# Performance work log

Measured on AMD Instinct MI355X. Metric: run time of the kernel, lower is better.

Reference implementation:

```python
import jax, jax.numpy as jnp
import numpy as np

RADIUS = 0.25
N_SAMPLE = 4096
N_NEIGHBOR = 32
OFF = 512   # voxel-coordinate offset so hashed coords are non-negative
M = 1024    # per-axis range of the voxel hash


def _bin_map():
    # 3^3 = 27 neighbor voxel offsets in {-1,0,1}^3 (Point2Voxel.extract_bin for D=3)
    g = np.stack(np.meshgrid(*([[-1, 0, 1]] * 3), indexing='ij'), -1).reshape(-1, 3)
    return jnp.asarray(g, dtype=jnp.int32)


def _hash(k):
    # k: [..., 3] int32 voxel coords -> unique int32 key (fits: 1024^3 < 2^31)
    return ((k[..., 0] + OFF) * M + (k[..., 1] + OFF)) * M + (k[..., 2] + OFF)


def setup_inputs() -> dict:
    key = jax.random.key(0)
    k1, k2 = jax.random.split(key)
    pos = jax.random.normal(k1, (8, 100000, 3), jnp.float32)
    feat = jax.random.normal(k2, (8, 100000, 64), jnp.float32)
    return {"pos": pos, "feat": feat}


def _graph_one(pos_b, rk):
    """Voxel-hash based neighbor sampling for one point cloud [N,3]."""
    N = pos_b.shape[0]
    vox = jnp.floor(pos_b / RADIUS).astype(jnp.int32)          # [N,3] voxel keys
    hkeys = _hash(vox)                                          # [N]
    order = jnp.argsort(hkeys)                                  # sort points by voxel (hash table)
    skeys = hkeys[order]
    kc, kn = jax.random.split(rk)
    centers = jax.random.randint(kc, (N_SAMPLE,), 0, N)         # sampled center point ids
    nk = _hash(vox[centers][:, None, :] + _bin_map()[None])     # [S,27] neighbor voxel keys
    lo = jnp.searchsorted(skeys, nk, side='left')               # bucket start  [S,27]
    hi = jnp.searchsorted(skeys, nk, side='right')              # bucket end    [S,27]
    counts = hi - lo                                            # bucket sizes
    cum = jnp.cumsum(counts, axis=1)                            # [S,27]
    total = cum[:, -1]                                          # candidates per center (>=1)
    # sample N_NEIGHBOR candidate slots uniformly over all neighbor-voxel points
    r = jax.random.randint(kn, (N_SAMPLE, N_NEIGHBOR), 0, 1 << 30) % total[:, None]
    slot = (r[:, :, None] >= cum[:, None, :]).sum(-1)           # which of the 27 voxels
    cum_ex = jnp.concatenate([jnp.zeros_like(cum[:, :1]), cum[:, :-1]], axis=1)
    prev = jnp.take_along_axis(cum_ex, slot, axis=1)
    start = jnp.take_along_axis(lo, slot, axis=1)
    src = order[start + (r - prev)]                             # [S,K] source point ids
    return centers, src


def reference(pos, feat):
    B, N, D = pos.shape
    C = feat.shape[-1]
    rks = jax.random.split(jax.random.key(42), B)
    centers, src = jax.vmap(_graph_one)(pos, rks)               # [B,S], [B,S,K]
    bidx = jnp.arange(B)[:, None]
    center_flag = jnp.zeros((B, N), pos.dtype).at[bidx, centers].set(1.0)
    src_flag = jnp.zeros((B, N), pos.dtype).at[bidx, src.reshape(B, -1)].set(1.0)
    b3 = jnp.arange(B)[:, None, None]
    pos_src = pos[b3, src]                                      # [B,S,K,3] gather
    pos_ctr = pos[bidx, centers]                                # [B,S,3]
    rel = pos_src - pos_ctr[:, :, None, :]                      # edge geometry
    f_src = feat[b3, src]                                       # [B,S,K,C] gather
    out = jnp.concatenate([rel, f_src], axis=-1)                # [B,S,K,3+C]
    return out, src, centers, center_flag, src_flag
```

## Files before the change

### kernel.cpp

```cpp
#include <hip/hip_runtime.h>
#include <stdint.h>

#define NB 8
#define NPTS 100000
#define NS 4096
#define NN 32
#define NCH 64
#define TLG 17
#define TSLOTS (1 << TLG)
#define TMASK (TSLOTS - 1)

#define OUT_MAIN 0ull
#define OUT_SRC  70254592ull
#define OUT_CTR  71303168ull
#define OUT_CF   71335936ull
#define OUT_SF   72135936ull

__host__ __device__ static inline uint32_t rotl32(uint32_t v, int d) {
    return (v << d) | (v >> (32 - d));
}

__host__ __device__ static inline void tf2x32(uint32_t k0, uint32_t k1,
                                              uint32_t x0, uint32_t x1,
                                              uint32_t& o0, uint32_t& o1) {
    uint32_t ks2 = k0 ^ k1 ^ 0x1BD11BDAu;
    x0 += k0; x1 += k1;
    x0 += x1; x1 = rotl32(x1, 13); x1 ^= x0;
    x0 += x1; x1 = rotl32(x1, 15); x1 ^= x0;
    x0 += x1; x1 = rotl32(x1, 26); x1 ^= x0;
    x0 += x1; x1 = rotl32(x1, 6);  x1 ^= x0;
    x0 += k1; x1 += ks2 + 1u;
    x0 += x1; x1 = rotl32(x1, 17); x1 ^= x0;
    x0 += x1; x1 = rotl32(x1, 29); x1 ^= x0;
    x0 += x1; x1 = rotl32(x1, 16); x1 ^= x0;
    x0 += x1; x1 = rotl32(x1, 24); x1 ^= x0;
    x0 += ks2; x1 += k0 + 2u;
    x0 += x1; x1 = rotl32(x1, 13); x1 ^= x0;
    x0 += x1; x1 = rotl32(x1, 15); x1 ^= x0;
    x0 += x1; x1 = rotl32(x1, 26); x1 ^= x0;
    x0 += x1; x1 = rotl32(x1, 6);  x1 ^= x0;
    x0 += k0; x1 += k1 + 3u;
    x0 += x1; x1 = rotl32(x1, 17); x1 ^= x0;
    x0 += x1; x1 = rotl32(x1, 29); x1 ^= x0;
    x0 += x1; x1 = rotl32(x1, 16); x1 ^= x0;
    x0 += x1; x1 = rotl32(x1, 24); x1 ^= x0;
    x0 += k1; x1 += ks2 + 4u;
    x0 += x1; x1 = rotl32(x1, 13); x1 ^= x0;
    x0 += x1; x1 = rotl32(x1, 15); x1 ^= x0;
    x0 += x1; x1 = rotl32(x1, 26); x1 ^= x0;
    x0 += x1; x1 = rotl32(x1, 6);  x1 ^= x0;
    x0 += ks2; x1 += k0 + 5u;
    o0 = x0; o1 = x1;
}

struct RngKeys {
    uint32_t c0[NB], c1[NB];
    uint32_t n0[NB], n1[NB];
};

__device__ static inline uint32_t pbits32(uint32_t k0, uint32_t k1, uint32_t u) {
    uint32_t o0, o1;
    tf2x32(k0, k1, 0u, u, o0, o1);
    return o0 ^ o1;
}

__device__ static inline int voxhash(const float* __restrict__ p) {
    int vx = (int)floorf(p[0] * 4.0f);
    int vy = (int)floorf(p[1] * 4.0f);
    int vz = (int)floorf(p[2] * 4.0f);
    return ((vx + 512) << 20) | ((vy + 512) << 10) | (vz + 512);
}

__device__ static inline int hslot(int hk) {
    return (int)(((uint32_t)hk * 2654435761u) >> (32 - TLG)) & TMASK;
}

__global__ void k_zero(int* __restrict__ tab_key, int* __restrict__ tab_cnt,
                       int* __restrict__ bctr, float4* __restrict__ flags4) {
    int t = blockIdx.x * blockDim.x + threadIdx.x;
    tab_key[t] = -1;
    tab_cnt[t] = 0;
    if (t < (2 * NB * NPTS) / 4) flags4[t] = make_float4(0.f, 0.f, 0.f, 0.f);
    if (t < NB) bctr[t] = 0;
}

__global__ void k_insert(const float* __restrict__ pos,
                         int* __restrict__ tab_key, int* __restrict__ tab_cnt,
                         int* __restrict__ slotOf) {
    int t = blockIdx.x * blockDim.x + threadIdx.x;
    int b = t / NPTS;
    int hk = voxhash(pos + (size_t)t * 3);
    int base = b << TLG;
    int slot = hslot(hk);
    while (true) {
        int prev = atomicCAS(&tab_key[base + slot], -1, hk);
        if (prev == -1 || prev == hk) break;
        slot = (slot + 1) & TMASK;
    }
    slotOf[t] = slot;
    atomicAdd(&tab_cnt[base + slot], 1);
}

__global__ void k_starts(int* __restrict__ tab_cnt, int* __restrict__ tab_start,
                         int* __restrict__ bctr) {
    __shared__ int sdata[256];
    __shared__ int sbase;
    int t = blockIdx.x * blockDim.x + threadIdx.x;
    int tid = threadIdx.x;
    int b = t >> TLG;
    int c = tab_cnt[t];
    sdata[tid] = c;
    __syncthreads();
    for (int off = 1; off < 256; off <<= 1) {
        int x = (tid >= off) ? sdata[tid - off] : 0;
        __syncthreads();
        sdata[tid] += x;
        __syncthreads();
    }
    if (tid == 255) sbase = atomicAdd(&bctr[b], sdata[255]);
    __syncthreads();
    if (c > 0) {
        tab_start[t] = sbase + sdata[tid] - c;
        tab_cnt[t] = 0;
    }
}

__global__ void k_scatter(const int* __restrict__ slotOf, int* __restrict__ tab_cnt,
                          const int* __restrict__ tab_start, int* __restrict__ listA) {
    int t = blockIdx.x * blockDim.x + threadIdx.x;
    int b = t / NPTS, i = t - b * NPTS;
    int slot = (b << TLG) + slotOf[t];
    int a = atomicAdd(&tab_cnt[slot], 1);
    listA[(size_t)b * NPTS + tab_start[slot] + a] = i;
}

__global__ void k_rank(const int* __restrict__ slotOf,
                       const int* __restrict__ tab_cnt, const int* __restrict__ tab_start,
                       const int* __restrict__ listA, int* __restrict__ listB) {
    int t = blockIdx.x * blockDim.x + threadIdx.x;
    int b = t / NPTS, i = t - b * NPTS;
    int slot = (b << TLG) + slotOf[t];
    int s0 = tab_start[slot];
    int c = tab_cnt[slot];
    const int* L = listA + (size_t)b * NPTS + s0;
    int rank = 0;
    for (int k = 0; k < c; k++) rank += (L[k] < i) ? 1 : 0;
    listB[(size_t)b * NPTS + s0 + rank] = i;
}

__global__ void k_binsel(RngKeys keys, const float* __restrict__ pos,
                         const int* __restrict__ tab_key, const int* __restrict__ tab_cnt,
                         const int* __restrict__ tab_start,
                         int* __restrict__ centers_ws,
                         int* __restrict__ lo_ws, int* __restrict__ cnt_ws,
                         float* __restrict__ out_ctr, float* __restrict__ out_cf) {
    int t = blockIdx.x * blockDim.x + threadIdx.x;
    int bin = t % 27;
    int bs = t / 27;
    int b = bs >> 12, s = bs & (NS - 1);
    uint32_t lower = pbits32(keys.c0[b], keys.c1[b], (uint32_t)s);
    int c = (int)(lower % 100000u);
    const float* p = pos + ((size_t)b * NPTS + c) * 3;
    int hk = voxhash(p) + ((bin / 9) - 1) * (1 << 20)
                        + (((bin / 3) % 3) - 1) * (1 << 10)
                        + ((bin % 3) - 1);
    int base = b << TLG;
    int slot = hslot(hk);
    int lo = 0, cnt = 0;
    while (true) {
        int k = tab_key[base + slot];
        if (k == hk) { lo = tab_start[base + slot]; cnt = tab_cnt[base + slot]; break; }
        if (k == -1) break;
        slot = (slot + 1) & TMASK;
    }
    lo_ws[t] = lo;
    cnt_ws[t] = cnt;
    if (bin == 13) {
        centers_ws[bs] = c;
        out_ctr[bs] = (float)c;
        out_cf[(size_t)b * NPTS + c] = 1.0f;
    }
}

__global__ void k_cumsel(RngKeys keys, const int* __restrict__ listB,
                         const int* __restrict__ lo_ws, const int* __restrict__ cnt_ws,
                         int* __restrict__ src_ws,
                         float* __restrict__ out_src, float* __restrict__ out_sf) {
    __shared__ int scnt[216];
    __shared__ int slo[216];
    int tid = threadIdx.x;
    int base216 = blockIdx.x * 216;
    if (tid < 216) {
        scnt[tid] = cnt_ws[base216 + tid];
        slo[tid]  = lo_ws[base216 + tid];
    }
    __syncthreads();
    if (tid < 8) {
        int* a = scnt + tid * 27;
        int acc = 0;
        for (int i = 0; i < 27; i++) { acc += a[i]; a[i] = acc; }
    }
    __syncthreads();
    int g = tid >> 5, n = tid & 31;
    int bs = blockIdx.x * 8 + g;
    int b = bs >> 12, s = bs & (NS - 1);
    uint32_t lower = pbits32(keys.n0[b], keys.n1[b], (uint32_t)(s * NN + n));
    const int* cum = scnt + g * 27;
    int total = cum[26];
    int r = (int)(lower & 0x3FFFFFFFu) % total;
    int slot = 0, prev = 0;
    #pragma unroll
    for (int i = 0; i < 27; i++) {
        int ci = cum[i];
        if (r >= ci) { slot = i + 1; prev = ci; }
    }
    int pos_in = slo[g * 27 + slot] + (r - prev);
    int src = listB[(size_t)b * NPTS + pos_in];
    int oi = bs * NN + n;
    src_ws[oi] = src;
    out_src[oi] = (float)src;
    out_sf[(size_t)b * NPTS + src] = 1.0f;
}

__global__ void k_gather(const float* __restrict__ pos, const float* __restrict__ feat,
                         const int* __restrict__ centers_ws, const int* __restrict__ src_ws,
                         float* __restrict__ out) {
    __shared__ float sbuf[16 * 67];
    int t = threadIdx.x;
    int g = t >> 4, q = t & 15;
    long long row0 = (long long)blockIdx.x * 16;
    long long row = row0 + g;
    int b = (int)(row >> 17);
    int u = (int)(row & (NS * NN - 1));
    int s = u >> 5;
    int src = src_ws[row];
    const float4 fv = *(const float4*)(feat + ((size_t)b * NPTS + src) * NCH + 4 * q);
    float* sb = sbuf + g * 67;
    sb[3 + 4 * q + 0] = fv.x;
    sb[3 + 4 * q + 1] = fv.y;
    sb[3 + 4 * q + 2] = fv.z;
    sb[3 + 4 * q + 3] = fv.w;
    if (q < 3) {
        int ctr = centers_ws[b * NS + s];
        sb[q] = pos[((size_t)b * NPTS + src) * 3 + q]
              - pos[((size_t)b * NPTS + ctr) * 3 + q];
    }
    __syncthreads();
    float4* ob = (float4*)(out + (size_t)row0 * 67);
    const float4* sv = (const float4*)sbuf;
    ob[t] = sv[t];
    if (t < 12) ob[256 + t] = sv[256 + t];
}

extern "C" void kernel_launch(void* const* d_in, const int* in_sizes, int n_in,
                              void* d_out, int out_size, void* d_ws, size_t ws_size,
                              hipStream_t stream) {
    (void)in_sizes; (void)n_in; (void)out_size; (void)ws_size;
    const float* pos = (const float*)d_in[0];
    const float* feat = (const float*)d_in[1];
    float* out = (float*)d_out;

    RngKeys keys;
    for (int b = 0; b < NB; b++) {
        uint32_t rk0, rk1, kc0, kc1, kn0, kn1;
        tf2x32(0u, 42u, 0u, (uint32_t)b, rk0, rk1);
        tf2x32(rk0, rk1, 0u, 0u, kc0, kc1);
        tf2x32(rk0, rk1, 0u, 1u, kn0, kn1);
        tf2x32(kc0, kc1, 0u, 1u, keys.c0[b], keys.c1[b]);
        tf2x32(kn0, kn1, 0u, 1u, keys.n0[b], keys.n1[b]);
    }

    int* tab_key    = (int*)d_ws;
    int* tab_cnt    = tab_key + (size_t)NB * TSLOTS;
    int* tab_start  = tab_cnt + (size_t)NB * TSLOTS;
    int* bctr       = tab_start + (size_t)NB * TSLOTS;
    int* slotOf     = bctr + NB;
    int* listA      = slotOf + (size_t)NB * NPTS;
    int* listB      = listA + (size_t)NB * NPTS;
    int* lo_ws      = listB + (size_t)NB * NPTS;
    int* cnt_ws     = lo_ws + (size_t)NB * NS * 27;
    int* centers_ws = cnt_ws + (size_t)NB * NS * 27;
    int* src_ws     = centers_ws + (size_t)NB * NS;

    k_zero   <<<(NB * TSLOTS) / 256, 256, 0, stream>>>(tab_key, tab_cnt, bctr,
                                                       (float4*)(out + OUT_CF));
    k_insert <<<(NB * NPTS) / 256, 256, 0, stream>>>(pos, tab_key, tab_cnt, slotOf);
    k_starts <<<(NB * TSLOTS) / 256, 256, 0, stream>>>(tab_cnt, tab_start, bctr);
    k_scatter<<<(NB * NPTS) / 256, 256, 0, stream>>>(slotOf, tab_cnt, tab_start, listA);
    k_rank   <<<(NB * NPTS) / 256, 256, 0, stream>>>(slotOf, tab_cnt, tab_start,
                                                     listA, listB);
    k_binsel <<<(NB * NS * 27) / 256, 256, 0, stream>>>(keys, pos, tab_key, tab_cnt,
                                                        tab_start, centers_ws,
                                                        lo_ws, cnt_ws,
                                                        out + OUT_CTR, out + OUT_CF);
    k_cumsel <<<(NB * NS) / 8, 256, 0, stream>>>(keys, listB, lo_ws, cnt_ws,
                                                 src_ws, out + OUT_SRC, out + OUT_SF);
    k_gather <<<(NB * NS * NN) / 16, 256, 0, stream>>>(pos, feat, centers_ws, src_ws, out);
}
```

Baseline: 417.0 us.

## Fuse bin lookup into neighbor selection and widen gather with nontemporal stores

The hash-bin lookup kernel and the cumulative-selection kernel are merged into one kernel. Each 32-lane group now probes the 27 neighbor voxels itself, keeps the counts and starts in shared memory, and takes the prefix inline, so the lo/cnt workspace round trip and one launch go away. The gather kernel now handles 32 rows per 512-thread block and writes its output with nontemporal stores, aiming to reduce cache pollution from the large streaming write. In exchange, each thread in the fused kernel recomputes the running sum over 27 entries.

```diff
diff --git a/kernel.cpp b/kernel.cpp
--- a/kernel.cpp
+++ b/kernel.cpp
@@ -15,6 +15,8 @@
 #define OUT_CTR  71303168ull
 #define OUT_CF   71335936ull
 #define OUT_SF   72135936ull
+
+typedef float f32x4 __attribute__((ext_vector_type(4)));
 
 __host__ __device__ static inline uint32_t rotl32(uint32_t v, int d) {
     return (v << d) | (v >> (32 - d));
@@ -148,73 +150,56 @@
     listB[(size_t)b * NPTS + s0 + rank] = i;
 }
 
-__global__ void k_binsel(RngKeys keys, const float* __restrict__ pos,
-                         const int* __restrict__ tab_key, const int* __restrict__ tab_cnt,
-                         const int* __restrict__ tab_start,
-                         int* __restrict__ centers_ws,
-                         int* __restrict__ lo_ws, int* __restrict__ cnt_ws,
-                         float* __restrict__ out_ctr, float* __restrict__ out_cf) {
-    int t = blockIdx.x * blockDim.x + threadIdx.x;
-    int bin = t % 27;
-    int bs = t / 27;
+__global__ void k_sel(RngKeys keys, const float* __restrict__ pos,
+                      const int* __restrict__ tab_key, const int* __restrict__ tab_cnt,
+                      const int* __restrict__ tab_start, const int* __restrict__ listB,
+                      int* __restrict__ centers_ws, int* __restrict__ src_ws,
+                      float* __restrict__ out_ctr, float* __restrict__ out_cf,
+                      float* __restrict__ out_src, float* __restrict__ out_sf) {
+    __shared__ int scnt[8][27];
+    __shared__ int slo[8][27];
+    int tid = threadIdx.x;
+    int g = tid >> 5, n = tid & 31;
+    int bs = blockIdx.x * 8 + g;
     int b = bs >> 12, s = bs & (NS - 1);
-    uint32_t lower = pbits32(keys.c0[b], keys.c1[b], (uint32_t)s);
-    int c = (int)(lower % 100000u);
+    uint32_t lower_c = pbits32(keys.c0[b], keys.c1[b], (uint32_t)s);
+    int c = (int)(lower_c % 100000u);
     const float* p = pos + ((size_t)b * NPTS + c) * 3;
-    int hk = voxhash(p) + ((bin / 9) - 1) * (1 << 20)
-                        + (((bin / 3) % 3) - 1) * (1 << 10)
-                        + ((bin % 3) - 1);
-    int base = b << TLG;
-    int slot = hslot(hk);
-    int lo = 0, cnt = 0;
-    while (true) {
-        int k = tab_key[base + slot];
-        if (k == hk) { lo = tab_start[base + slot]; cnt = tab_cnt[base + slot]; break; }
-        if (k == -1) break;
-        slot = (slot + 1) & TMASK;
-    }
-    lo_ws[t] = lo;
-    cnt_ws[t] = cnt;
-    if (bin == 13) {
+    int chk = voxhash(p);
+    if (n < 27) {
+        int hk = chk + ((n / 9) - 1) * (1 << 20)
+                     + (((n / 3) % 3) - 1) * (1 << 10)
+                     + ((n % 3) - 1);
+        int base = b << TLG;
+        int slot = hslot(hk);
+        int lo = 0, cnt = 0;
+        while (true) {
+            int k = tab_key[base + slot];
+            if (k == hk) { lo = tab_start[base + slot]; cnt = tab_cnt[base + slot]; break; }
+            if (k == -1) break;
+            slot = (slot + 1) & TMASK;
+        }
+        scnt[g][n] = cnt;
+        slo[g][n] = lo;
+    }
+    if (n == 0) {
         centers_ws[bs] = c;
         out_ctr[bs] = (float)c;
         out_cf[(size_t)b * NPTS + c] = 1.0f;
     }
-}
-
-__global__ void k_cumsel(RngKeys keys, const int* __restrict__ listB,
-                         const int* __restrict__ lo_ws, const int* __restrict__ cnt_ws,
-                         int* __restrict__ src_ws,
-                         float* __restrict__ out_src, float* __restrict__ out_sf) {
-    __shared__ int scnt[216];
-    __shared__ int slo[216];
-    int tid = threadIdx.x;
-    int base216 = blockIdx.x * 216;
-    if (tid < 216) {
-        scnt[tid] = cnt_ws[base216 + tid];
-        slo[tid]  = lo_ws[base216 + tid];
-    }
-    __syncthreads();
-    if (tid < 8) {
-        int* a = scnt + tid * 27;
-        int acc = 0;
-        for (int i = 0; i < 27; i++) { acc += a[i]; a[i] = acc; }
-    }
-    __syncthreads();
-    int g = tid >> 5, n = tid & 31;
-    int bs = blockIdx.x * 8 + g;
-    int b = bs >> 12, s = bs & (NS - 1);
+    __syncthreads();
     uint32_t lower = pbits32(keys.n0[b], keys.n1[b], (uint32_t)(s * NN + n));
-    const int* cum = scnt + g * 27;
-    int total = cum[26];
+    int total = 0;
+    #pragma unroll
+    for (int i = 0; i < 27; i++) total += scnt[g][i];
     int r = (int)(lower & 0x3FFFFFFFu) % total;
-    int slot = 0, prev = 0;
+    int slot = 0, prev = 0, acc = 0;
     #pragma unroll
     for (int i = 0; i < 27; i++) {
-        int ci = cum[i];
-        if (r >= ci) { slot = i + 1; prev = ci; }
-    }
-    int pos_in = slo[g * 27 + slot] + (r - prev);
+        acc += scnt[g][i];
+        if (r >= acc) { slot = i + 1; prev = acc; }
+    }
+    int pos_in = slo[g][slot] + (r - prev);
     int src = listB[(size_t)b * NPTS + pos_in];
     int oi = bs * NN + n;
     src_ws[oi] = src;
@@ -225,10 +210,10 @@
 __global__ void k_gather(const float* __restrict__ pos, const float* __restrict__ feat,
                          const int* __restrict__ centers_ws, const int* __restrict__ src_ws,
                          float* __restrict__ out) {
-    __shared__ float sbuf[16 * 67];
+    __shared__ float sbuf[32 * 67];
     int t = threadIdx.x;
     int g = t >> 4, q = t & 15;
-    long long row0 = (long long)blockIdx.x * 16;
+    long long row0 = (long long)blockIdx.x * 32;
     long long row = row0 + g;
     int b = (int)(row >> 17);
     int u = (int)(row & (NS * NN - 1));
@@ -246,10 +231,10 @@
               - pos[((size_t)b * NPTS + ctr) * 3 + q];
     }
     __syncthreads();
-    float4* ob = (float4*)(out + (size_t)row0 * 67);
-    const float4* sv = (const float4*)sbuf;
-    ob[t] = sv[t];
-    if (t < 12) ob[256 + t] = sv[256 + t];
+    f32x4* ob = (f32x4*)(out + (size_t)row0 * 67);
+    const f32x4* sv = (const f32x4*)sbuf;
+    __builtin_nontemporal_store(sv[t], &ob[t]);
+    if (t < 24) __builtin_nontemporal_store(sv[512 + t], &ob[512 + t]);
 }
 
 extern "C" void kernel_launch(void* const* d_in, const int* in_sizes, int n_in,
@@ -277,9 +262,7 @@
     int* slotOf     = bctr + NB;
     int* listA      = slotOf + (size_t)NB * NPTS;
     int* listB      = listA + (size_t)NB * NPTS;
-    int* lo_ws      = listB + (size_t)NB * NPTS;
-    int* cnt_ws     = lo_ws + (size_t)NB * NS * 27;
-    int* centers_ws = cnt_ws + (size_t)NB * NS * 27;
+    int* centers_ws = listB + (size_t)NB * NPTS;
     int* src_ws     = centers_ws + (size_t)NB * NS;
 
     k_zero   <<<(NB * TSLOTS) / 256, 256, 0, stream>>>(tab_key, tab_cnt, bctr,
@@ -289,11 +272,9 @@
     k_scatter<<<(NB * NPTS) / 256, 256, 0, stream>>>(slotOf, tab_cnt, tab_start, listA);
     k_rank   <<<(NB * NPTS) / 256, 256, 0, stream>>>(slotOf, tab_cnt, tab_start,
                                                      listA, listB);
-    k_binsel <<<(NB * NS * 27) / 256, 256, 0, stream>>>(keys, pos, tab_key, tab_cnt,
-                                                        tab_start, centers_ws,
-                                                        lo_ws, cnt_ws,
-                                                        out + OUT_CTR, out + OUT_CF);
-    k_cumsel <<<(NB * NS) / 8, 256, 0, stream>>>(keys, listB, lo_ws, cnt_ws,
-                                                 src_ws, out + OUT_SRC, out + OUT_SF);
-    k_gather <<<(NB * NS * NN) / 16, 256, 0, stream>>>(pos, feat, centers_ws, src_ws, out);
-}
+    k_sel    <<<(NB * NS) / 8, 256, 0, stream>>>(keys, pos, tab_key, tab_cnt, tab_start,
+                                                 listB, centers_ws, src_ws,
+                                                 out + OUT_CTR, out + OUT_CF,
+                                                 out + OUT_SRC, out + OUT_SF);
+    k_gather <<<(NB * NS * NN) / 32, 512, 0, stream>>>(pos, feat, centers_ws, src_ws, out);
+}
```

Result: faster. 364.2 us (-12.7%).
